# Performance work log

Hardware: AMD Instinct MI355X
Metric: run time of the kernel (lower is better)

## Reference

```python
import jax, jax.numpy as jnp
import numpy as np

GROUPS = 1  # module-level groups arg


def adaptive_avg_pool(x, out_size):
    # Equal-tile average pool (exact match to torch AdaptiveAvgPool2d when H,W divisible by out_size)
    b, c, h, w = x.shape
    fh, fw = h // out_size, w // out_size
    return x.reshape(b, c, out_size, fh, out_size, fw).mean(axis=(3, 5))


def setup_inputs() -> dict:
    key = jax.random.key(0)
    k1, k2, k3, k4 = jax.random.split(key, 4)
    x = jax.random.normal(k1, (64, 128, 80, 80), jnp.float32)
    weight = jax.random.normal(k2, (128, 128, 3, 3), jnp.float32) * 0.05   # static conv weight [out, icg, k, k]
    w_att = jax.random.normal(k3, (16384, 1, 3, 3), jnp.float32) * 0.05    # conv_att weight (groups=icg=128)
    b_att = jax.random.normal(k4, (16384,), jnp.float32) * 0.05            # conv_att bias
    return {"x": x, "weight": weight, "w_att": w_att, "b_att": b_att}


def reference(x, weight, w_att, b_att):
    b, cin, h, w = x.shape
    out_ch, icg, k, _ = weight.shape  # icg = in_channels // groups
    pad = 1

    # attention branch: adaptive avg pool to (k+2), grouped 3x3 VALID conv -> [b, out*icg, k, k]
    avg = adaptive_avg_pool(x, k + 2)
    att = jax.lax.conv_general_dilated(avg, w_att, (1, 1), "VALID",
                                       feature_group_count=icg)
    att = jax.nn.sigmoid(att + b_att[None, :, None, None])
    att = att.reshape(b, out_ch, icg, k, k)

    # per-sample dynamic kernels
    dyn_w = weight[None] * att                    # [b, out, icg, k, k]

    # batch-grouped conv: fold batch into channels, groups = b * GROUPS
    xg = x.reshape(1, b * cin, h, w)
    wg = dyn_w.reshape(b * out_ch, icg, k, k)
    out = jax.lax.conv_general_dilated(xg, wg, (1, 1), [(pad, pad), (pad, pad)],
                                       feature_group_count=b * GROUPS)
    return out.reshape(b, out_ch, out.shape[-2], out.shape[-1])
```

## Files before the change

kernel.cpp:

```cpp
#include <hip/hip_runtime.h>

typedef __bf16 bf16;
typedef __bf16 bf16x8 __attribute__((ext_vector_type(8)));
typedef float f32x4 __attribute__((ext_vector_type(4)));

#define NB 64
#define NC 128
#define NOC 128
#define HW 80
#define HPAD 82

#define XT_BYTES  110166016L
#define W2_BYTES  18874368L
#define AVG_BYTES 819200L
#define WS_NEEDED (XT_BYTES + W2_BYTES + AVG_BYTES)

__global__ void pool_kernel(const float* __restrict__ x, float* __restrict__ avg) {
    int wave = (blockIdx.x * blockDim.x + threadIdx.x) >> 6;
    int lane = threadIdx.x & 63;
    int j = wave % 5; int t = wave / 5;
    int i = t % 5; t /= 5;
    int c = t & 127; int b = t >> 7;
    const float* src = x + (((long)(b * 128 + c) * 80) + i * 16) * 80 + j * 16;
    int ry = lane >> 2;
    int rx = (lane & 3) * 4;
    float4 v = *reinterpret_cast<const float4*>(src + ry * 80 + rx);
    float s = v.x + v.y + v.z + v.w;
    #pragma unroll
    for (int off = 32; off > 0; off >>= 1) s += __shfl_down(s, off, 64);
    if (lane == 0) avg[wave] = s * (1.0f / 256.0f);
}

__global__ void transpose_kernel(const float* __restrict__ x, bf16* __restrict__ xT) {
    __shared__ bf16 tile[64 * 68];
    int b = blockIdx.z, icb = blockIdx.y, pxb = blockIdx.x;
    int t = threadIdx.x;
    int pl = t & 63;
    int ig = t >> 6;
    const float* src = x + ((long)(b * 128 + icb * 64) * 6400) + pxb * 64;
    #pragma unroll
    for (int it = 0; it < 16; ++it) {
        int ic = ig * 16 + it;
        float v = src[(long)ic * 6400 + pl];
        tile[pl * 68 + ic] = (bf16)v;
    }
    __syncthreads();
    #pragma unroll
    for (int it = 0; it < 4; ++it) {
        int idx = it * 256 + t;
        int pxl = idx >> 4;
        int icq = idx & 15;
        int px = pxb * 64 + pxl;
        int Y = px / 80 + 1, X = px % 80 + 1;
        uint2 v = *reinterpret_cast<const uint2*>(&tile[pxl * 68 + icq * 4]);
        *reinterpret_cast<uint2*>(&xT[(((long)b * 82 + Y) * 82 + X) * 128 + icb * 64 + icq * 4]) = v;
    }
}

__global__ void att_kernel(const float* __restrict__ avg, const float* __restrict__ weight,
                           const float* __restrict__ w_att, const float* __restrict__ b_att,
                           bf16* __restrict__ W2) {
    __shared__ float sa[25];
    int b = blockIdx.x >> 7, och = blockIdx.x & 127;
    int ic = threadIdx.x;
    if (ic < 25) sa[ic] = avg[(long)blockIdx.x * 25 + ic];
    __syncthreads();
    int o = och * 128 + ic;
    float wa[9];
    #pragma unroll
    for (int j = 0; j < 9; ++j) wa[j] = w_att[(long)o * 9 + j];
    float bias = b_att[o];
    const float* wst = weight + (long)o * 9;
    #pragma unroll
    for (int kh = 0; kh < 3; ++kh) {
        #pragma unroll
        for (int kw = 0; kw < 3; ++kw) {
            float z = bias;
            #pragma unroll
            for (int di = 0; di < 3; ++di)
                #pragma unroll
                for (int dj = 0; dj < 3; ++dj)
                    z += sa[(kh + di) * 5 + (kw + dj)] * wa[di * 3 + dj];
            float s = 1.0f / (1.0f + __expf(-z));
            float dw = wst[kh * 3 + kw] * s;
            int p = kh * 3 + kw;
            W2[(((long)b * 9 + p) * 128 + och) * 128 + ic] = (bf16)dw;
        }
    }
}

__global__ __launch_bounds__(256, 2)
void conv_gemm(const bf16* __restrict__ xT, const bf16* __restrict__ W2,
               float* __restrict__ out) {
    __shared__ bf16 Xs[180 * 128];
    __shared__ bf16 Ws[128 * 64];
    int b = blockIdx.z;
    int px0 = blockIdx.x * 16;
    int py0 = blockIdx.y * 8;
    int t = threadIdx.x;
    int wave = t >> 6, lane = t & 63;
    int q = lane >> 4;
    int li = lane & 15;

    {
        const bf16* src = xT + (((long)b * 82 + py0) * 82 + px0) * 128;
        #pragma unroll
        for (int it = 0; it < 12; ++it) {
            int idx = it * 256 + t;
            if (idx < 2880) {
                int pf = idx >> 4, icb = idx & 15;
                int r = pf / 18, cx = pf - r * 18;
                uint4 v = *reinterpret_cast<const uint4*>(src + ((long)r * 82 + cx) * 128 + icb * 8);
                *reinterpret_cast<uint4*>(&Xs[pf * 128 + ((icb ^ (pf & 7)) * 8)]) = v;
            }
        }
    }

    f32x4 acc[4][4];
    #pragma unroll
    for (int i = 0; i < 4; ++i)
        #pragma unroll
        for (int j = 0; j < 4; ++j) acc[i][j] = (f32x4){0.f, 0.f, 0.f, 0.f};

    int ow = (wave >> 1) * 64;
    int nw = (wave & 1) * 64;

    for (int p = 0; p < 9; ++p) {
        int kh = p / 3, kw = p - kh * 3;
        for (int h = 0; h < 2; ++h) {
            __syncthreads();
            {
                const bf16* wsrc = W2 + ((long)b * 9 + p) * 128 * 128 + h * 64;
                #pragma unroll
                for (int it = 0; it < 4; ++it) {
                    int idx = it * 256 + t;
                    int och = idx >> 3, icb = idx & 7;
                    uint4 v = *reinterpret_cast<const uint4*>(wsrc + och * 128 + icb * 8);
                    *reinterpret_cast<uint4*>(&Ws[och * 64 + ((icb ^ (och & 7)) * 8)]) = v;
                }
            }
            __syncthreads();
            #pragma unroll
            for (int k2 = 0; k2 < 2; ++k2) {
                int ic0 = k2 * 32;
                bf16x8 af[4], bfr[4];
                #pragma unroll
                for (int mi = 0; mi < 4; ++mi) {
                    int och = ow + mi * 16 + li;
                    int icb = (ic0 >> 3) + q;
                    af[mi] = *reinterpret_cast<const bf16x8*>(&Ws[och * 64 + ((icb ^ (och & 7)) * 8)]);
                }
                #pragma unroll
                for (int ni = 0; ni < 4; ++ni) {
                    int n = nw + ni * 16 + li;
                    int oy = n >> 4, ox = n & 15;
                    int pf = (oy + kh) * 18 + ox + kw;
                    int icbx = h * 8 + (ic0 >> 3) + q;
                    bfr[ni] = *reinterpret_cast<const bf16x8*>(&Xs[pf * 128 + ((icbx ^ (pf & 7)) * 8)]);
                }
                #pragma unroll
                for (int mi = 0; mi < 4; ++mi)
                    #pragma unroll
                    for (int ni = 0; ni < 4; ++ni)
                        acc[mi][ni] = __builtin_amdgcn_mfma_f32_16x16x32_bf16(af[mi], bfr[ni], acc[mi][ni], 0, 0, 0);
            }
        }
    }

    #pragma unroll
    for (int mi = 0; mi < 4; ++mi) {
        #pragma unroll
        for (int ni = 0; ni < 4; ++ni) {
            int n = nw + ni * 16 + li;
            int oy = py0 + (n >> 4), ox = px0 + (n & 15);
            #pragma unroll
            for (int r = 0; r < 4; ++r) {
                int och = ow + mi * 16 + q * 4 + r;
                out[((long)(b * 128 + och) * 80 + oy) * 80 + ox] = acc[mi][ni][r];
            }
        }
    }
}

extern "C" void kernel_launch(void* const* d_in, const int* in_sizes, int n_in,
                              void* d_out, int out_size, void* d_ws, size_t ws_size,
                              hipStream_t stream) {
    const float* x      = (const float*)d_in[0];
    const float* weight = (const float*)d_in[1];
    const float* w_att  = (const float*)d_in[2];
    const float* b_att  = (const float*)d_in[3];
    float* out = (float*)d_out;

    if (ws_size < (size_t)WS_NEEDED) return;

    char* ws = (char*)d_ws;
    bf16* xT  = (bf16*)ws;
    bf16* W2  = (bf16*)(ws + XT_BYTES);
    float* avg = (float*)(ws + XT_BYTES + W2_BYTES);

    hipMemsetAsync(xT, 0, XT_BYTES, stream);

    pool_kernel<<<51200, 256, 0, stream>>>(x, avg);
    transpose_kernel<<<dim3(100, 2, 64), 256, 0, stream>>>(x, xT);
    att_kernel<<<8192, 128, 0, stream>>>(avg, weight, w_att, b_att, W2);
    conv_gemm<<<dim3(5, 10, 64), 256, 0, stream>>>(xT, W2, out);
}
```

Baseline: 566.5 us.

## Zero only halo, pool from bf16 transposed input, double-buffer async weight loads with 32x32 MFMA

```diff
diff --git a/kernel.cpp b/kernel.cpp
--- a/kernel.cpp
+++ b/kernel.cpp
@@ -2,37 +2,45 @@
 
 typedef __bf16 bf16;
 typedef __bf16 bf16x8 __attribute__((ext_vector_type(8)));
-typedef float f32x4 __attribute__((ext_vector_type(4)));
+typedef float f32x16 __attribute__((ext_vector_type(16)));
 
 #define NB 64
 #define NC 128
-#define NOC 128
 #define HW 80
-#define HPAD 82
 
 #define XT_BYTES  110166016L
 #define W2_BYTES  18874368L
 #define AVG_BYTES 819200L
 #define WS_NEEDED (XT_BYTES + W2_BYTES + AVG_BYTES)
 
-__global__ void pool_kernel(const float* __restrict__ x, float* __restrict__ avg) {
-    int wave = (blockIdx.x * blockDim.x + threadIdx.x) >> 6;
-    int lane = threadIdx.x & 63;
-    int j = wave % 5; int t = wave / 5;
-    int i = t % 5; t /= 5;
-    int c = t & 127; int b = t >> 7;
-    const float* src = x + (((long)(b * 128 + c) * 80) + i * 16) * 80 + j * 16;
-    int ry = lane >> 2;
-    int rx = (lane & 3) * 4;
-    float4 v = *reinterpret_cast<const float4*>(src + ry * 80 + rx);
-    float s = v.x + v.y + v.z + v.w;
-    #pragma unroll
-    for (int off = 32; off > 0; off >>= 1) s += __shfl_down(s, off, 64);
-    if (lane == 0) avg[wave] = s * (1.0f / 256.0f);
+__device__ __forceinline__ void async16(const void* g, void* l) {
+    __builtin_amdgcn_global_load_lds((const __attribute__((address_space(1))) void*)g,
+                                     (__attribute__((address_space(3))) void*)l, 16, 0, 0);
+}
+
+__global__ void zero_halo(bf16* __restrict__ xT) {
+    int b = blockIdx.x;
+    long base = (long)b * 82 * 82 * 128;
+    uint4 z = make_uint4(0u, 0u, 0u, 0u);
+    for (int k = threadIdx.x; k < 5184; k += 256) {
+        long off;
+        if (k < 1312) {
+            off = (long)k * 8;
+        } else if (k < 2624) {
+            off = (long)81 * 82 * 128 + (long)(k - 1312) * 8;
+        } else {
+            int r = k - 2624;
+            int Y = (r >> 5) + 1;
+            int side = (r >> 4) & 1;
+            int cq = r & 15;
+            off = ((long)Y * 82 + side * 81) * 128 + cq * 8;
+        }
+        *reinterpret_cast<uint4*>(xT + base + off) = z;
+    }
 }
 
 __global__ void transpose_kernel(const float* __restrict__ x, bf16* __restrict__ xT) {
-    __shared__ bf16 tile[64 * 68];
+    __shared__ __align__(16) bf16 tile[64 * 68];
     int b = blockIdx.z, icb = blockIdx.y, pxb = blockIdx.x;
     int t = threadIdx.x;
     int pl = t & 63;
@@ -54,6 +62,34 @@
         int Y = px / 80 + 1, X = px % 80 + 1;
         uint2 v = *reinterpret_cast<const uint2*>(&tile[pxl * 68 + icq * 4]);
         *reinterpret_cast<uint2*>(&xT[(((long)b * 82 + Y) * 82 + X) * 128 + icb * 64 + icq * 4]) = v;
+    }
+}
+
+__global__ void pool_kernel(const bf16* __restrict__ xT, float* __restrict__ avg) {
+    __shared__ float part[256][8];
+    int bid = blockIdx.x;
+    int j = bid % 5; int t2 = bid / 5; int i = t2 % 5; int b = t2 / 5;
+    int t = threadIdx.x;
+    int pxg = t >> 4, cc = t & 15;
+    const bf16* src = xT + (((long)b * 82 + 1 + i * 16) * 82 + 1 + j * 16 + pxg) * 128 + cc * 8;
+    float s[8];
+    #pragma unroll
+    for (int e = 0; e < 8; ++e) s[e] = 0.f;
+    #pragma unroll
+    for (int dy = 0; dy < 16; ++dy) {
+        bf16x8 v = *reinterpret_cast<const bf16x8*>(src + (long)dy * 82 * 128);
+        #pragma unroll
+        for (int e = 0; e < 8; ++e) s[e] += (float)v[e];
+    }
+    #pragma unroll
+    for (int e = 0; e < 8; ++e) part[t][e] = s[e];
+    __syncthreads();
+    if (t < 128) {
+        int cc2 = t >> 3, e = t & 7;
+        float sum = 0.f;
+        #pragma unroll
+        for (int g = 0; g < 16; ++g) sum += part[g * 16 + cc2][e];
+        avg[(((long)b * 128 + cc2 * 8 + e) * 5 + i) * 5 + j] = sum * (1.0f / 256.0f);
     }
 }
 
@@ -92,91 +128,103 @@
 __global__ __launch_bounds__(256, 2)
 void conv_gemm(const bf16* __restrict__ xT, const bf16* __restrict__ W2,
                float* __restrict__ out) {
-    __shared__ bf16 Xs[180 * 128];
-    __shared__ bf16 Ws[128 * 64];
+    __shared__ __align__(16) bf16 Xs[180 * 128];
+    __shared__ __align__(16) bf16 Ws[2][128 * 64];
     int b = blockIdx.z;
     int px0 = blockIdx.x * 16;
     int py0 = blockIdx.y * 8;
     int t = threadIdx.x;
     int wave = t >> 6, lane = t & 63;
-    int q = lane >> 4;
-    int li = lane & 15;
-
-    {
-        const bf16* src = xT + (((long)b * 82 + py0) * 82 + px0) * 128;
-        #pragma unroll
-        for (int it = 0; it < 12; ++it) {
-            int idx = it * 256 + t;
-            if (idx < 2880) {
-                int pf = idx >> 4, icb = idx & 15;
-                int r = pf / 18, cx = pf - r * 18;
-                uint4 v = *reinterpret_cast<const uint4*>(src + ((long)r * 82 + cx) * 128 + icb * 8);
-                *reinterpret_cast<uint4*>(&Xs[pf * 128 + ((icb ^ (pf & 7)) * 8)]) = v;
-            }
-        }
-    }
-
-    f32x4 acc[4][4];
-    #pragma unroll
-    for (int i = 0; i < 4; ++i)
-        #pragma unroll
-        for (int j = 0; j < 4; ++j) acc[i][j] = (f32x4){0.f, 0.f, 0.f, 0.f};
-
+    int l31 = lane & 31, hl = lane >> 5;
     int ow = (wave >> 1) * 64;
     int nw = (wave & 1) * 64;
 
-    for (int p = 0; p < 9; ++p) {
+    {
+        const bf16* xsrc = xT + (((long)b * 82 + py0) * 82 + px0) * 128;
+        for (int cidx = wave; cidx < 45; cidx += 4) {
+            int idx0 = cidx << 6;
+            int idx = idx0 + lane;
+            int pf = idx >> 4, icb = idx & 15;
+            int r = pf / 18, cx = pf - r * 18;
+            async16(xsrc + ((long)r * 82 + cx) * 128 + ((icb ^ (pf & 7)) << 3),
+                    &Xs[idx0 * 8]);
+        }
+        const bf16* wsrc = W2 + (long)b * 9 * 16384;
+        #pragma unroll
+        for (int it = 0; it < 4; ++it) {
+            int idx0 = it * 256 + (wave << 6);
+            int idx = idx0 + lane;
+            int och = idx >> 3, icb = idx & 7;
+            async16(wsrc + och * 128 + ((icb ^ (och & 7)) << 3), &Ws[0][idx0 * 8]);
+        }
+    }
+    asm volatile("s_waitcnt vmcnt(0)" ::: "memory");
+    __builtin_amdgcn_s_barrier();
+    asm volatile("" ::: "memory");
+
+    f32x16 acc[2][2];
+    #pragma unroll
+    for (int mi = 0; mi < 2; ++mi)
+        #pragma unroll
+        for (int ni = 0; ni < 2; ++ni)
+            #pragma unroll
+            for (int r = 0; r < 16; ++r) acc[mi][ni][r] = 0.f;
+
+    int aRow0 = (ow + l31) * 64;
+    int sA = l31 & 7;
+    int pfb = ((nw + l31) >> 4) * 18 + ((nw + l31) & 15);
+
+    #pragma unroll
+    for (int tt = 0; tt < 18; ++tt) {
+        int p = tt >> 1, h = tt & 1;
         int kh = p / 3, kw = p - kh * 3;
-        for (int h = 0; h < 2; ++h) {
-            __syncthreads();
-            {
-                const bf16* wsrc = W2 + ((long)b * 9 + p) * 128 * 128 + h * 64;
-                #pragma unroll
-                for (int it = 0; it < 4; ++it) {
-                    int idx = it * 256 + t;
-                    int och = idx >> 3, icb = idx & 7;
-                    uint4 v = *reinterpret_cast<const uint4*>(wsrc + och * 128 + icb * 8);
-                    *reinterpret_cast<uint4*>(&Ws[och * 64 + ((icb ^ (och & 7)) * 8)]) = v;
-                }
+        if (tt < 17) {
+            int p2 = (tt + 1) >> 1, h2 = (tt + 1) & 1;
+            const bf16* wsrc = W2 + ((long)b * 9 + p2) * 16384 + h2 * 64;
+            bf16* ldst = &Ws[(tt + 1) & 1][0];
+            #pragma unroll
+            for (int it = 0; it < 4; ++it) {
+                int idx0 = it * 256 + (wave << 6);
+                int idx = idx0 + lane;
+                int och = idx >> 3, icb = idx & 7;
+                async16(wsrc + och * 128 + ((icb ^ (och & 7)) << 3), ldst + idx0 * 8);
             }
-            __syncthreads();
-            #pragma unroll
-            for (int k2 = 0; k2 < 2; ++k2) {
-                int ic0 = k2 * 32;
-                bf16x8 af[4], bfr[4];
-                #pragma unroll
-                for (int mi = 0; mi < 4; ++mi) {
-                    int och = ow + mi * 16 + li;
-                    int icb = (ic0 >> 3) + q;
-                    af[mi] = *reinterpret_cast<const bf16x8*>(&Ws[och * 64 + ((icb ^ (och & 7)) * 8)]);
-                }
-                #pragma unroll
-                for (int ni = 0; ni < 4; ++ni) {
-                    int n = nw + ni * 16 + li;
-                    int oy = n >> 4, ox = n & 15;
-                    int pf = (oy + kh) * 18 + ox + kw;
-                    int icbx = h * 8 + (ic0 >> 3) + q;
-                    bfr[ni] = *reinterpret_cast<const bf16x8*>(&Xs[pf * 128 + ((icbx ^ (pf & 7)) * 8)]);
-                }
-                #pragma unroll
-                for (int mi = 0; mi < 4; ++mi)
-                    #pragma unroll
-                    for (int ni = 0; ni < 4; ++ni)
-                        acc[mi][ni] = __builtin_amdgcn_mfma_f32_16x16x32_bf16(af[mi], bfr[ni], acc[mi][ni], 0, 0, 0);
-            }
-        }
-    }
-
-    #pragma unroll
-    for (int mi = 0; mi < 4; ++mi) {
-        #pragma unroll
-        for (int ni = 0; ni < 4; ++ni) {
-            int n = nw + ni * 16 + li;
+        }
+        const bf16* Wb = &Ws[tt & 1][0];
+        __builtin_amdgcn_s_setprio(1);
+        #pragma unroll
+        for (int ks = 0; ks < 4; ++ks) {
+            int icb = ks * 2 + hl;
+            bf16x8 a0 = *reinterpret_cast<const bf16x8*>(Wb + aRow0 + ((icb ^ sA) << 3));
+            bf16x8 a1 = *reinterpret_cast<const bf16x8*>(Wb + aRow0 + 2048 + ((icb ^ sA) << 3));
+            int icbx = h * 8 + icb;
+            int pf0 = pfb + kh * 18 + kw;
+            int pf1 = pf0 + 36;
+            bf16x8 b0 = *reinterpret_cast<const bf16x8*>(&Xs[pf0 * 128 + ((icbx ^ (pf0 & 7)) << 3)]);
+            bf16x8 b1 = *reinterpret_cast<const bf16x8*>(&Xs[pf1 * 128 + ((icbx ^ (pf1 & 7)) << 3)]);
+            acc[0][0] = __builtin_amdgcn_mfma_f32_32x32x16_bf16(a0, b0, acc[0][0], 0, 0, 0);
+            acc[0][1] = __builtin_amdgcn_mfma_f32_32x32x16_bf16(a0, b1, acc[0][1], 0, 0, 0);
+            acc[1][0] = __builtin_amdgcn_mfma_f32_32x32x16_bf16(a1, b0, acc[1][0], 0, 0, 0);
+            acc[1][1] = __builtin_amdgcn_mfma_f32_32x32x16_bf16(a1, b1, acc[1][1], 0, 0, 0);
+        }
+        __builtin_amdgcn_s_setprio(0);
+        __builtin_amdgcn_sched_barrier(0);
+        asm volatile("s_waitcnt vmcnt(0)" ::: "memory");
+        __builtin_amdgcn_s_barrier();
+        asm volatile("" ::: "memory");
+    }
+
+    #pragma unroll
+    for (int mi = 0; mi < 2; ++mi) {
+        #pragma unroll
+        for (int ni = 0; ni < 2; ++ni) {
+            int n = nw + ni * 32 + l31;
             int oy = py0 + (n >> 4), ox = px0 + (n & 15);
-            #pragma unroll
-            for (int r = 0; r < 4; ++r) {
-                int och = ow + mi * 16 + q * 4 + r;
-                out[((long)(b * 128 + och) * 80 + oy) * 80 + ox] = acc[mi][ni][r];
+            float* ob = out + ((long)(b * 128 + ow + mi * 32 + 4 * hl) * 80 + oy) * 80 + ox;
+            #pragma unroll
+            for (int reg = 0; reg < 16; ++reg) {
+                int row = (reg & 3) + 8 * (reg >> 2);
+                ob[(long)row * 6400] = acc[mi][ni][reg];
             }
         }
     }
@@ -198,10 +246,9 @@
     bf16* W2  = (bf16*)(ws + XT_BYTES);
     float* avg = (float*)(ws + XT_BYTES + W2_BYTES);
 
-    hipMemsetAsync(xT, 0, XT_BYTES, stream);
-
-    pool_kernel<<<51200, 256, 0, stream>>>(x, avg);
+    zero_halo<<<64, 256, 0, stream>>>(xT);
     transpose_kernel<<<dim3(100, 2, 64), 256, 0, stream>>>(x, xT);
+    pool_kernel<<<1600, 256, 0, stream>>>(xT, avg);
     att_kernel<<<8192, 128, 0, stream>>>(avg, weight, w_att, b_att, W2);
     conv_gemm<<<dim3(5, 10, 64), 256, 0, stream>>>(xT, W2, out);
 }
```

Result: faster. 521.5 us (-7.9%).
